# Performance work log

Hardware: AMD Instinct MI355X
Metric: run time of the kernel (lower is better)

The kernel has to match this reference:

```python
import jax, jax.numpy as jnp
import numpy as np

H = 16  # n_head

def _rotate_half(x):
    d = x.shape[-1] // 2
    return jnp.concatenate([-x[..., d:], x[..., :d]], axis=-1)

def setup_inputs() -> dict:
    key = jax.random.key(0)
    ks = jax.random.split(key, 12)
    b, t, f, h = 8, 1024, 1024, H
    d = f // h
    inp = {
        "query": jax.random.normal(ks[0], (b, t, f), jnp.float32),
        "key": jax.random.normal(ks[1], (b, t, f), jnp.float32),
        "value": jax.random.normal(ks[2], (b, t, f), jnp.float32),
    }
    # realistic rotary cos/sin, shape (t,1,1,d_k)
    inv_freq = 1.0 / (10000.0 ** (np.arange(0, d, 2, dtype=np.float32) / d))
    pos = np.arange(t, dtype=np.float32)[:, None] * inv_freq[None, :]  # (t, d/2)
    emb = np.concatenate([pos, pos], axis=-1)  # (t, d)
    inp["cos"] = jnp.asarray(np.cos(emb)).reshape(t, 1, 1, d)
    inp["sin"] = jnp.asarray(np.sin(emb)).reshape(t, 1, 1, d)
    inp["mask"] = jax.random.randint(ks[3], (b, t, t), 0, 2) > 0
    s = 1.0 / np.sqrt(f)
    inp["Wq"] = jax.random.normal(ks[4], (f, f), jnp.float32) * s
    inp["bq"] = jax.random.normal(ks[5], (f,), jnp.float32) * 0.02
    inp["Wk"] = jax.random.normal(ks[6], (f, f), jnp.float32) * s
    inp["bk"] = jax.random.normal(ks[7], (f,), jnp.float32) * 0.02
    inp["Wv"] = jax.random.normal(ks[8], (f, f), jnp.float32) * s
    inp["bv"] = jax.random.normal(ks[9], (f,), jnp.float32) * 0.02
    inp["Wo"] = jax.random.normal(ks[10], (f, f), jnp.float32) * s
    inp["bo"] = jax.random.normal(ks[11], (f,), jnp.float32) * 0.02
    return inp

def reference(query, key, value, cos, sin, mask, Wq, bq, Wk, bk, Wv, bv, Wo, bo):
    b, t, f = query.shape
    h = H
    d = f // h
    # RoPE applied pre-projection, per-head layout (b,t,h,d)
    c = cos.reshape(1, t, 1, d)  # broadcast over batch and heads
    s = sin.reshape(1, t, 1, d)
    qr = query.reshape(b, t, h, d)
    kr = key.reshape(b, t, h, d)
    qr = qr * c + _rotate_half(qr) * s
    kr = kr * c + _rotate_half(kr) * s
    q_in = qr.reshape(b, t, f)
    k_in = kr.reshape(b, t, f)
    # QKV projections (nn.Linear: x @ W.T + b), then split heads -> (b,h,t,d)
    q = (jnp.einsum('btf,gf->btg', q_in, Wq) + bq).reshape(b, t, h, d).transpose(0, 2, 1, 3)
    k = (jnp.einsum('btf,gf->btg', k_in, Wk) + bk).reshape(b, t, h, d).transpose(0, 2, 1, 3)
    v = (jnp.einsum('btf,gf->btg', value, Wv) + bv).reshape(b, t, h, d).transpose(0, 2, 1, 3)
    scores = jnp.einsum('bhqd,bhkd->bhqk', q, k) / jnp.sqrt(jnp.asarray(d, q.dtype))
    m = mask[:, None, :, :]  # (b,1,t,t)
    scores = jnp.where(m, jnp.asarray(-10000.0, scores.dtype), scores)
    attn = jax.nn.softmax(scores, axis=-1)
    attn = jnp.where(m, jnp.asarray(0.0, attn.dtype), attn)
    out = jnp.einsum('bhqk,bhkd->bhqd', attn, v)  # (b,h,t,d)
    out = out.transpose(0, 2, 1, 3).reshape(b, t, f)
    return jnp.einsum('btf,gf->btg', out, Wo) + bo
```

## Files before the change

kernel.cpp:

```cpp
#include <hip/hip_runtime.h>
#include <stdint.h>

typedef short short8 __attribute__((ext_vector_type(8)));
typedef float f32x4 __attribute__((ext_vector_type(4)));
typedef unsigned short ushort4v __attribute__((ext_vector_type(4)));
typedef unsigned int uint4v __attribute__((ext_vector_type(4)));
typedef unsigned long long u64;
typedef u64 u64x2 __attribute__((ext_vector_type(2)));

#if __has_builtin(__builtin_amdgcn_exp2f)
#define EXP2(x) __builtin_amdgcn_exp2f(x)
#else
#define EXP2(x) exp2f(x)
#endif

__device__ __forceinline__ unsigned short f2bf(float f) {
  union { float f; unsigned u; } v; v.f = f;
  unsigned r = v.u + 0x7fffu + ((v.u >> 16) & 1u);
  return (unsigned short)(r >> 16);
}

__device__ __forceinline__ unsigned cvt_pk_bf16(float lo, float hi) {
  unsigned r;
  asm("v_cvt_pk_bf16_f32 %0, %1, %2" : "=v"(r) : "v"(lo), "v"(hi));
  return r;
}

__device__ __forceinline__ void gld_lds16(const void* g, void* l) {
  __builtin_amdgcn_global_load_lds((const __attribute__((address_space(1))) void*)g,
                                   (__attribute__((address_space(3))) void*)l, 16, 0, 0);
}

__device__ __forceinline__ unsigned nib_compress(u64 x) {
  x = (x | (x >> 4))  & 0x00FF00FF00FF00FFull;
  x = (x | (x >> 8))  & 0x0000FFFF0000FFFFull;
  x = (x | (x >> 16));
  return (unsigned)x;
}

__device__ __forceinline__ void cast32(const float* __restrict__ src,
                                       unsigned short* __restrict__ dst) {
  const float4 a = *(const float4*)(src);
  const float4 b = *(const float4*)(src + 4);
  const float4 c = *(const float4*)(src + 8);
  const float4 d = *(const float4*)(src + 12);
  const float4 e = *(const float4*)(src + 16);
  const float4 f = *(const float4*)(src + 20);
  const float4 g = *(const float4*)(src + 24);
  const float4 h = *(const float4*)(src + 28);
  uint4v o0, o1, o2, o3;
  o0[0] = cvt_pk_bf16(a.x, a.y); o0[1] = cvt_pk_bf16(a.z, a.w);
  o0[2] = cvt_pk_bf16(b.x, b.y); o0[3] = cvt_pk_bf16(b.z, b.w);
  o1[0] = cvt_pk_bf16(c.x, c.y); o1[1] = cvt_pk_bf16(c.z, c.w);
  o1[2] = cvt_pk_bf16(d.x, d.y); o1[3] = cvt_pk_bf16(d.z, d.w);
  o2[0] = cvt_pk_bf16(e.x, e.y); o2[1] = cvt_pk_bf16(e.z, e.w);
  o2[2] = cvt_pk_bf16(f.x, f.y); o2[3] = cvt_pk_bf16(f.z, f.w);
  o3[0] = cvt_pk_bf16(g.x, g.y); o3[1] = cvt_pk_bf16(g.z, g.w);
  o3[2] = cvt_pk_bf16(h.x, h.y); o3[3] = cvt_pk_bf16(h.z, h.w);
  *(uint4v*)(dst)      = o0;
  *(uint4v*)(dst + 8)  = o1;
  *(uint4v*)(dst + 16) = o2;
  *(uint4v*)(dst + 24) = o3;
}

__global__ void prep_kernel(const float* __restrict__ q, const float* __restrict__ k,
                            const float* __restrict__ v,
                            const float* __restrict__ cs, const float* __restrict__ sn,
                            unsigned short* __restrict__ qo, unsigned short* __restrict__ ko,
                            unsigned short* __restrict__ vo,
                            const int* __restrict__ mask, u64* __restrict__ bits,
                            const float* __restrict__ s0, const float* __restrict__ s1,
                            const float* __restrict__ s2, const float* __restrict__ s3,
                            unsigned short* __restrict__ d0, unsigned short* __restrict__ d1,
                            unsigned short* __restrict__ d2, unsigned short* __restrict__ d3) {
  __shared__ unsigned mlds[256];
  const int tid = threadIdx.x;
  const int bx = blockIdx.x;
  if (bx < 1024) {
    const int idx  = bx * 256 + tid;
    const int half = idx & 1;
    const int row  = idx >> 1;
    const int t    = (row >> 4) & 1023;
    const size_t base = (size_t)row * 64 + half * 16;
    const int coff = t * 64 + half * 16;

    const float4 ca = *(const float4*)(cs + coff);
    const float4 cb = *(const float4*)(cs + coff + 4);
    const float4 cc = *(const float4*)(cs + coff + 8);
    const float4 cd = *(const float4*)(cs + coff + 12);
    const float4 sa = *(const float4*)(sn + coff);
    const float4 sb = *(const float4*)(sn + coff + 4);
    const float4 sc = *(const float4*)(sn + coff + 8);
    const float4 sd = *(const float4*)(sn + coff + 12);
    const float4 x0a = *(const float4*)(q + base);
    const float4 x0b = *(const float4*)(q + base + 4);
    const float4 x0c = *(const float4*)(q + base + 8);
    const float4 x0d = *(const float4*)(q + base + 12);
    const float4 x1a = *(const float4*)(q + base + 32);
    const float4 x1b = *(const float4*)(q + base + 36);
    const float4 x1c = *(const float4*)(q + base + 40);
    const float4 x1d = *(const float4*)(q + base + 44);
    const float4 y0a = *(const float4*)(k + base);
    const float4 y0b = *(const float4*)(k + base + 4);
    const float4 y0c = *(const float4*)(k + base + 8);
    const float4 y0d = *(const float4*)(k + base + 12);
    const float4 y1a = *(const float4*)(k + base + 32);
    const float4 y1b = *(const float4*)(k + base + 36);
    const float4 y1c = *(const float4*)(k + base + 40);
    const float4 y1d = *(const float4*)(k + base + 44);

    uint4v qlo0, qlo1, qhi0, qhi1;
    qlo0[0] = cvt_pk_bf16(x0a.x*ca.x - x1a.x*sa.x, x0a.y*ca.y - x1a.y*sa.y);
    qlo0[1] = cvt_pk_bf16(x0a.z*ca.z - x1a.z*sa.z, x0a.w*ca.w - x1a.w*sa.w);
    qlo0[2] = cvt_pk_bf16(x0b.x*cb.x - x1b.x*sb.x, x0b.y*cb.y - x1b.y*sb.y);
    qlo0[3] = cvt_pk_bf16(x0b.z*cb.z - x1b.z*sb.z, x0b.w*cb.w - x1b.w*sb.w);
    qlo1[0] = cvt_pk_bf16(x0c.x*cc.x - x1c.x*sc.x, x0c.y*cc.y - x1c.y*sc.y);
    qlo1[1] = cvt_pk_bf16(x0c.z*cc.z - x1c.z*sc.z, x0c.w*cc.w - x1c.w*sc.w);
    qlo1[2] = cvt_pk_bf16(x0d.x*cd.x - x1d.x*sd.x, x0d.y*cd.y - x1d.y*sd.y);
    qlo1[3] = cvt_pk_bf16(x0d.z*cd.z - x1d.z*sd.z, x0d.w*cd.w - x1d.w*sd.w);
    qhi0[0] = cvt_pk_bf16(x1a.x*ca.x + x0a.x*sa.x, x1a.y*ca.y + x0a.y*sa.y);
    qhi0[1] = cvt_pk_bf16(x1a.z*ca.z + x0a.z*sa.z, x1a.w*ca.w + x0a.w*sa.w);
    qhi0[2] = cvt_pk_bf16(x1b.x*cb.x + x0b.x*sb.x, x1b.y*cb.y + x0b.y*sb.y);
    qhi0[3] = cvt_pk_bf16(x1b.z*cb.z + x0b.z*sb.z, x1b.w*cb.w + x0b.w*sb.w);
    qhi1[0] = cvt_pk_bf16(x1c.x*cc.x + x0c.x*sc.x, x1c.y*cc.y + x0c.y*sc.y);
    qhi1[1] = cvt_pk_bf16(x1c.z*cc.z + x0c.z*sc.z, x1c.w*cc.w + x0c.w*sc.w);
    qhi1[2] = cvt_pk_bf16(x1d.x*cd.x + x0d.x*sd.x, x1d.y*cd.y + x0d.y*sd.y);
    qhi1[3] = cvt_pk_bf16(x1d.z*cd.z + x0d.z*sd.z, x1d.w*cd.w + x0d.w*sd.w);
    *(uint4v*)(qo + base)      = qlo0;
    *(uint4v*)(qo + base + 8)  = qlo1;
    *(uint4v*)(qo + base + 32) = qhi0;
    *(uint4v*)(qo + base + 40) = qhi1;

    uint4v klo0, klo1, khi0, khi1;
    klo0[0] = cvt_pk_bf16(y0a.x*ca.x - y1a.x*sa.x, y0a.y*ca.y - y1a.y*sa.y);
    klo0[1] = cvt_pk_bf16(y0a.z*ca.z - y1a.z*sa.z, y0a.w*ca.w - y1a.w*sa.w);
    klo0[2] = cvt_pk_bf16(y0b.x*cb.x - y1b.x*sb.x, y0b.y*cb.y - y1b.y*sb.y);
    klo0[3] = cvt_pk_bf16(y0b.z*cb.z - y1b.z*sb.z, y0b.w*cb.w - y1b.w*sb.w);
    klo1[0] = cvt_pk_bf16(y0c.x*cc.x - y1c.x*sc.x, y0c.y*cc.y - y1c.y*sc.y);
    klo1[1] = cvt_pk_bf16(y0c.z*cc.z - y1c.z*sc.z, y0c.w*cc.w - y1c.w*sc.w);
    klo1[2] = cvt_pk_bf16(y0d.x*cd.x - y1d.x*sd.x, y0d.y*cd.y - y1d.y*sd.y);
    klo1[3] = cvt_pk_bf16(y0d.z*cd.z - y1d.z*sd.z, y0d.w*cd.w - y1d.w*sd.w);
    khi0[0] = cvt_pk_bf16(y1a.x*ca.x + y0a.x*sa.x, y1a.y*ca.y + y0a.y*sa.y);
    khi0[1] = cvt_pk_bf16(y1a.z*ca.z + y0a.z*sa.z, y1a.w*ca.w + y0a.w*sa.w);
    khi0[2] = cvt_pk_bf16(y1b.x*cb.x + y0b.x*sb.x, y1b.y*cb.y + y0b.y*sb.y);
    khi0[3] = cvt_pk_bf16(y1b.z*cb.z + y0b.z*sb.z, y1b.w*cb.w + y0b.w*sb.w);
    khi1[0] = cvt_pk_bf16(y1c.x*cc.x + y0c.x*sc.x, y1c.y*cc.y + y0c.y*sc.y);
    khi1[1] = cvt_pk_bf16(y1c.z*cc.z + y0c.z*sc.z, y1c.w*cc.w + y0c.w*sc.w);
    khi1[2] = cvt_pk_bf16(y1d.x*cd.x + y0d.x*sd.x, y1d.y*cd.y + y0d.y*sd.y);
    khi1[3] = cvt_pk_bf16(y1d.z*cd.z + y0d.z*sd.z, y1d.w*cd.w + y0d.w*sd.w);
    *(uint4v*)(ko + base)      = klo0;
    *(uint4v*)(ko + base + 8)  = klo1;
    *(uint4v*)(ko + base + 32) = khi0;
    *(uint4v*)(ko + base + 40) = khi1;
  } else if (bx < 2048) {
    const size_t off = ((size_t)(bx - 1024) * 256 + tid) * 32;
    cast32(v + off, vo + off);
  } else if (bx < 2560) {
    const int idx2 = bx - 2048;
    const int m = idx2 >> 7;
    const float* src = (m == 0) ? s0 : (m == 1) ? s1 : (m == 2) ? s2 : s3;
    unsigned short* dst = (m == 0) ? d0 : (m == 1) ? d1 : (m == 2) ? d2 : d3;
    const size_t off = ((size_t)(idx2 & 127) * 256 + tid) * 32;
    cast32(src + off, dst + off);
  } else {
    const int wave = tid >> 6, lane = tid & 63;
    const int mrow = (bx - 2560) * 4 + wave;
    const int* mp = mask + (size_t)mrow * 1024 + lane * 16;
    const int4 a0 = *(const int4*)(mp);
    const int4 a1 = *(const int4*)(mp + 4);
    const int4 a2 = *(const int4*)(mp + 8);
    const int4 a3 = *(const int4*)(mp + 12);
    const unsigned n0 = (a0.x!=0?1u:0u)|(a0.y!=0?2u:0u)|(a0.z!=0?4u:0u)|(a0.w!=0?8u:0u);
    const unsigned n1 = (a1.x!=0?1u:0u)|(a1.y!=0?2u:0u)|(a1.z!=0?4u:0u)|(a1.w!=0?8u:0u);
    const unsigned n2 = (a2.x!=0?1u:0u)|(a2.y!=0?2u:0u)|(a2.z!=0?4u:0u)|(a2.w!=0?8u:0u);
    const unsigned n3 = (a3.x!=0?1u:0u)|(a3.y!=0?2u:0u)|(a3.z!=0?4u:0u)|(a3.w!=0?8u:0u);
    mlds[wave * 64 + lane] = n0 | (n1 << 8) | (n2 << 16) | (n3 << 24);
    if (lane < 16) {
      const u64x2 x = ((const u64x2*)mlds)[wave * 16 + lane];
      const u64 w = (u64)nib_compress(x[0]) | ((u64)nib_compress(x[1]) << 32);
      bits[(size_t)mrow * 16 + lane] = w;
    }
  }
}

__global__ __launch_bounds__(256, 4) void gemm_qkv(
    const unsigned short* __restrict__ Aq, const unsigned short* __restrict__ Ak,
    const unsigned short* __restrict__ Av,
    const unsigned short* __restrict__ Bq, const unsigned short* __restrict__ Bk,
    const unsigned short* __restrict__ Bv,
    const float* __restrict__ bq, const float* __restrict__ bk, const float* __restrict__ bv,
    unsigned short* __restrict__ Cq, unsigned short* __restrict__ Ck,
    unsigned short* __restrict__ Cv) {
  constexpr int K = 1024;
  const int z = blockIdx.z;
  const unsigned short* A  = (z == 0) ? Aq : (z == 1) ? Ak : Av;
  const unsigned short* Bw = (z == 0) ? Bq : (z == 1) ? Bk : Bv;
  const float* bias        = (z == 0) ? bq : (z == 1) ? bk : bv;
  unsigned short* Co       = (z == 0) ? Cq : (z == 1) ? Ck : Cv;
  const float scale = (z == 0) ? 0.18033688f : 1.0f;

  const int tid = threadIdx.x;
  const int wave = tid >> 6, lane = tid & 63;
  const int m0 = blockIdx.x * 128, n0 = blockIdx.y * 128;
  __shared__ unsigned short Asm[128 * 64];
  __shared__ unsigned short Bsm[128 * 64];
  f32x4 acc[4][4] = {};
  const int wr = (wave >> 1) * 64, wc = (wave & 1) * 64;
  const int ld_row = lane >> 3;
  const int ld_col = ((lane & 7) ^ ld_row) * 8;
  const int fr = lane & 15, g = lane >> 4;
  const int fr7 = fr & 7;

  for (int k0 = 0; k0 < K; k0 += 64) {
#pragma unroll
    for (int j = 0; j < 4; ++j) {
      const int c = j * 4 + wave;
      gld_lds16(A  + (size_t)(m0 + 8 * c + ld_row) * K + k0 + ld_col, &Asm[c * 512]);
      gld_lds16(Bw + (size_t)(n0 + 8 * c + ld_row) * K + k0 + ld_col, &Bsm[c * 512]);
    }
    __syncthreads();
#pragma unroll
    for (int ks = 0; ks < 2; ++ks) {
      const int ch = ((ks * 4 + g) ^ fr7) * 8;
      short8 af[4], bf[4];
#pragma unroll
      for (int i = 0; i < 4; ++i)
        af[i] = *(const short8*)&Asm[(wr + i * 16 + fr) * 64 + ch];
#pragma unroll
      for (int i = 0; i < 4; ++i)
        bf[i] = *(const short8*)&Bsm[(wc + i * 16 + fr) * 64 + ch];
#pragma unroll
      for (int i = 0; i < 4; ++i)
#pragma unroll
        for (int j = 0; j < 4; ++j)
          acc[i][j] = __builtin_amdgcn_mfma_f32_16x16x32_bf16(af[i], bf[j], acc[i][j], 0, 0, 0);
    }
    __syncthreads();
  }

#pragma unroll
  for (int i = 0; i < 4; ++i) {
    const int row_base = m0 + wr + i * 16 + g * 4;
#pragma unroll
    for (int j = 0; j < 4; ++j) {
      const int col = n0 + wc + j * 16 + fr;
      const float bval = bias[col];
      const int h_i = col >> 6, dd = col & 63;
      if (z < 2) {
#pragma unroll
        for (int r = 0; r < 4; ++r) {
          const int row = row_base + r;
          const int b_i = row >> 10, t_i = row & 1023;
          Co[((size_t)(b_i * 16 + h_i) * 1024 + t_i) * 64 + dd] = f2bf((acc[i][j][r] + bval) * scale);
        }
      } else {
#pragma unroll
        for (int r = 0; r < 4; ++r) {
          const int row = row_base + r;
          const int b_i = row >> 10, t_i = row & 1023;
          const int kk = t_i & 127;
          const int kp = ((kk >> 4) & 3) * 32 + ((kk >> 2) & 3) * 8 + ((kk >> 6) & 1) * 4 + (kk & 3);
          Co[((size_t)(b_i * 16 + h_i) * 64 + dd) * 1024 + (t_i & ~127) + kp] =
              f2bf((acc[i][j][r] + bval));
        }
      }
    }
  }
}

__global__ __launch_bounds__(256, 4) void gemm_o(
    const unsigned short* __restrict__ A, const unsigned short* __restrict__ Bw,
    const float* __restrict__ bias, float* __restrict__ C) {
  constexpr int K = 1024, N = 1024;
  const int tid = threadIdx.x;
  const int wave = tid >> 6, lane = tid & 63;
  const int m0 = blockIdx.x * 128, n0 = blockIdx.y * 128;
  __shared__ unsigned short Asm[128 * 64];
  __shared__ unsigned short Bsm[128 * 64];
  f32x4 acc[4][4] = {};
  const int wr = (wave >> 1) * 64, wc = (wave & 1) * 64;
  const int ld_row = lane >> 3;
  const int ld_col = ((lane & 7) ^ ld_row) * 8;
  const int fr = lane & 15, g = lane >> 4;
  const int fr7 = fr & 7;

  for (int k0 = 0; k0 < K; k0 += 64) {
#pragma unroll
    for (int j = 0; j < 4; ++j) {
      const int c = j * 4 + wave;
      gld_lds16(A  + (size_t)(m0 + 8 * c + ld_row) * K + k0 + ld_col, &Asm[c * 512]);
      gld_lds16(Bw + (size_t)(n0 + 8 * c + ld_row) * K + k0 + ld_col, &Bsm[c * 512]);
    }
    __syncthreads();
#pragma unroll
    for (int ks = 0; ks < 2; ++ks) {
      const int ch = ((ks * 4 + g) ^ fr7) * 8;
      short8 af[4], bf[4];
#pragma unroll
      for (int i = 0; i < 4; ++i)
        af[i] = *(const short8*)&Asm[(wr + i * 16 + fr) * 64 + ch];
#pragma unroll
      for (int i = 0; i < 4; ++i)
        bf[i] = *(const short8*)&Bsm[(wc + i * 16 + fr) * 64 + ch];
#pragma unroll
      for (int i = 0; i < 4; ++i)
#pragma unroll
        for (int j = 0; j < 4; ++j)
          acc[i][j] = __builtin_amdgcn_mfma_f32_16x16x32_bf16(af[i], bf[j], acc[i][j], 0, 0, 0);
    }
    __syncthreads();
  }

#pragma unroll
  for (int i = 0; i < 4; ++i) {
    const int row_base = m0 + wr + i * 16 + g * 4;
#pragma unroll
    for (int j = 0; j < 4; ++j) {
      const int col = n0 + wc + j * 16 + fr;
      const float bval = bias[col];
#pragma unroll
      for (int r = 0; r < 4; ++r)
        C[(size_t)(row_base + r) * N + col] = acc[i][j][r] + bval;
    }
  }
}

__global__ __launch_bounds__(256, 2) void flash_attn(
    const unsigned short* __restrict__ Qp, const unsigned short* __restrict__ Kp,
    const unsigned short* __restrict__ Vp, const u64* __restrict__ mbits,
    unsigned short* __restrict__ O) {
  const int bh = blockIdx.x & 127, b_i = bh >> 4, h_i = bh & 15;
  const int q0 = (blockIdx.x >> 7) * 128;
  const int tid = threadIdx.x, wave = tid >> 6, lane = tid & 63;
  const unsigned short* Qb = Qp + (size_t)bh * 65536;
  const unsigned short* Kb = Kp + (size_t)bh * 65536;
  const unsigned short* Vb = Vp + (size_t)bh * 65536;
  const u64* mb = mbits + (size_t)b_i * 16384;

  __shared__ unsigned short smem[32768];

  const int fr = lane & 15, g = lane >> 4, fr7 = fr & 7;
  const int shg = g * 4;
  const int qw = q0 + wave * 32;

  short8 qf[2][2];
#pragma unroll
  for (int mt = 0; mt < 2; ++mt)
#pragma unroll
    for (int ks = 0; ks < 2; ++ks)
      qf[mt][ks] = *(const short8*)&Qb[(size_t)(qw + mt * 16 + fr) * 64 + ks * 32 + g * 8];

  f32x4 o_acc[2][4] = {};
  f32x4 o_l[2] = {};
  const short8 ones = {0x3F80, 0x3F80, 0x3F80, 0x3F80, 0x3F80, 0x3F80, 0x3F80, 0x3F80};

  const int kld_row = lane >> 3;
  const int kld_col = ((lane & 7) ^ kld_row) * 8;
  const int vld_row = lane >> 4;
  const int vld_r7w = 4 * (wave & 1) + vld_row;
  const int vld_col = ((lane & 15) ^ vld_r7w) * 8;

#define STAGE(P, KT)                                                                     \
  do {                                                                                   \
    _Pragma("unroll")                                                                    \
    for (int j = 0; j < 4; ++j) {                                                        \
      const int c = j * 4 + wave;                                                        \
      gld_lds16(Kb + (size_t)((KT) + 8 * c + kld_row) * 64 + kld_col,                    \
                &smem[(P) * 16384 + 8192 + c * 512]);                                    \
      gld_lds16(Vb + (size_t)(4 * c + vld_row) * 1024 + (KT) + vld_col,                  \
                &smem[(P) * 16384 + c * 512]);                                           \
    }                                                                                    \
  } while (0)

  u64x2 wv0 = *(const u64x2*)&mb[(size_t)(qw + fr) * 16];
  u64x2 wv1 = *(const u64x2*)&mb[(size_t)(qw + 16 + fr) * 16];
  STAGE(0, 0);
  int p = 0;
  for (int kt = 0; kt < 1024; kt += 128) {
    if (kt < 896) {
      STAGE(p ^ 1, kt + 128);
      asm volatile("s_waitcnt vmcnt(8)" ::: "memory");
    } else {
      asm volatile("s_waitcnt vmcnt(0)" ::: "memory");
    }
    __builtin_amdgcn_s_barrier();
    asm volatile("" ::: "memory");
    const unsigned short* Vsm = &smem[p * 16384];
    const unsigned short* Ksm = &smem[p * 16384 + 8192];

    f32x4 s_acc[2][8] = {};
#pragma unroll
    for (int ks = 0; ks < 2; ++ks) {
      const int ch = ((ks * 4 + g) ^ fr7) * 8;
      short8 kf[8];
#pragma unroll
      for (int nt = 0; nt < 8; ++nt)
        kf[nt] = *(const short8*)&Ksm[(nt * 16 + fr) * 64 + ch];
      __builtin_amdgcn_s_setprio(1);
#pragma unroll
      for (int mt = 0; mt < 2; ++mt)
#pragma unroll
        for (int nt = 0; nt < 8; ++nt)
          s_acc[mt][nt] = __builtin_amdgcn_mfma_f32_16x16x32_bf16(kf[nt], qf[mt][ks], s_acc[mt][nt], 0, 0, 0);
      __builtin_amdgcn_s_setprio(0);
    }

    short8 pf[2][4];
#pragma unroll
    for (int mt = 0; mt < 2; ++mt) {
      const u64 sa = (mt ? wv1[0] : wv0[0]) >> shg;
      const u64 sb = (mt ? wv1[1] : wv0[1]) >> shg;
#pragma unroll
      for (int ks2 = 0; ks2 < 4; ++ks2) {
        float e[8];
#pragma unroll
        for (int r = 0; r < 4; ++r) {
          float a = EXP2(s_acc[mt][ks2][r]);
          a = ((unsigned)(sa >> (ks2 * 16 + r)) & 1u) ? 0.0f : a;
          float b2 = EXP2(s_acc[mt][ks2 + 4][r]);
          b2 = ((unsigned)(sb >> (ks2 * 16 + r)) & 1u) ? 0.0f : b2;
          e[r] = a; e[4 + r] = b2;
        }
        uint4v pk;
        pk[0] = cvt_pk_bf16(e[0], e[1]);
        pk[1] = cvt_pk_bf16(e[2], e[3]);
        pk[2] = cvt_pk_bf16(e[4], e[5]);
        pk[3] = cvt_pk_bf16(e[6], e[7]);
        union { uint4v u; short8 s; } cv; cv.u = pk;
        pf[mt][ks2] = cv.s;
      }
    }

    {
      const int ktn = (kt + 128) & 1023;
      wv0 = *(const u64x2*)&mb[(size_t)(qw + fr) * 16 + (ktn >> 6)];
      wv1 = *(const u64x2*)&mb[(size_t)(qw + 16 + fr) * 16 + (ktn >> 6)];
    }

#pragma unroll
    for (int ks2 = 0; ks2 < 4; ++ks2) {
      const int cc = (ks2 * 4 + g) ^ fr7;
      short8 vf[4];
#pragma unroll
      for (int dt = 0; dt < 4; ++dt)
        vf[dt] = *(const short8*)&Vsm[(dt * 16 + fr) * 128 + cc * 8];
      __builtin_amdgcn_s_setprio(1);
#pragma unroll
      for (int mt = 0; mt < 2; ++mt) {
#pragma unroll
        for (int dt = 0; dt < 4; ++dt)
          o_acc[mt][dt] = __builtin_amdgcn_mfma_f32_16x16x32_bf16(pf[mt][ks2], vf[dt], o_acc[mt][dt], 0, 0, 0);
        o_l[mt] = __builtin_amdgcn_mfma_f32_16x16x32_bf16(pf[mt][ks2], ones, o_l[mt], 0, 0, 0);
      }
      __builtin_amdgcn_s_setprio(0);
    }
    asm volatile("" ::: "memory");
    __builtin_amdgcn_s_barrier();
    p ^= 1;
  }
#undef STAGE

#pragma unroll
  for (int mt = 0; mt < 2; ++mt) {
#pragma unroll
    for (int r = 0; r < 4; ++r) {
      const float inv_l = 1.0f / o_l[mt][r];
      const int qrow = qw + mt * 16 + g * 4 + r;
#pragma unroll
      for (int dt = 0; dt < 4; ++dt) {
        const int dcol = dt * 16 + fr;
        O[((size_t)(b_i * 1024 + qrow)) * 1024 + h_i * 64 + dcol] = f2bf(o_acc[mt][dt][r] * inv_l);
      }
    }
  }
}

extern "C" void kernel_launch(void* const* d_in, const int* in_sizes, int n_in,
                              void* d_out, int out_size, void* d_ws, size_t ws_size,
                              hipStream_t stream) {
  const float* query = (const float*)d_in[0];
  const float* key   = (const float*)d_in[1];
  const float* value = (const float*)d_in[2];
  const float* cosb  = (const float*)d_in[3];
  const float* sinb  = (const float*)d_in[4];
  const int*   mask  = (const int*)d_in[5];
  const float* Wq = (const float*)d_in[6];
  const float* bq = (const float*)d_in[7];
  const float* Wk = (const float*)d_in[8];
  const float* bk = (const float*)d_in[9];
  const float* Wv = (const float*)d_in[10];
  const float* bv = (const float*)d_in[11];
  const float* Wo = (const float*)d_in[12];
  const float* bo = (const float*)d_in[13];
  (void)in_sizes; (void)n_in; (void)out_size; (void)ws_size;

  char* ws = (char*)d_ws;
  const size_t MB = 1024 * 1024;
  unsigned short* q_in = (unsigned short*)(ws);
  unsigned short* k_in = (unsigned short*)(ws + 16 * MB);
  unsigned short* v_bf = (unsigned short*)(ws + 32 * MB);
  unsigned short* Qp   = (unsigned short*)(ws + 48 * MB);
  unsigned short* Kp   = (unsigned short*)(ws + 64 * MB);
  unsigned short* Vp   = (unsigned short*)(ws + 80 * MB);
  unsigned short* Wqb  = (unsigned short*)(ws + 96 * MB);
  unsigned short* Wkb  = (unsigned short*)(ws + 98 * MB);
  unsigned short* Wvb  = (unsigned short*)(ws + 100 * MB);
  unsigned short* Wob  = (unsigned short*)(ws + 102 * MB);
  u64*            mbits= (u64*)(ws + 104 * MB);
  unsigned short* attn = q_in;

  prep_kernel<<<4608, 256, 0, stream>>>(query, key, value, cosb, sinb, q_in, k_in, v_bf,
                                        mask, mbits, Wq, Wk, Wv, Wo, Wqb, Wkb, Wvb, Wob);

  dim3 blk(256);
  gemm_qkv<<<dim3(64, 8, 3), blk, 0, stream>>>(q_in, k_in, v_bf, Wqb, Wkb, Wvb,
                                               bq, bk, bv, Qp, Kp, Vp);
  flash_attn<<<1024, blk, 0, stream>>>(Qp, Kp, Vp, mbits, attn);
  gemm_o<<<dim3(64, 8), blk, 0, stream>>>(attn, Wob, bo, (float*)d_out);
}
```

Measured before the change: 339.9 us.

## Double-buffer LDS tiles in QKV and output GEMMs with async prefetch

Both projection GEMMs now keep two LDS stages and issue the global-to-LDS loads for the next K tile before computing on the current one. Partial vmcnt waits and raw s_barrier replace the full __syncthreads, and setprio raises wave priority around the MFMA block. This is meant to hide global load latency behind matrix math. In exchange LDS use doubles, so occupancy is lowered to 2 blocks per CU, and the hand-counted vmcnt(8) has to match the number of outstanding loads issued per stage.

Measured after the change: 336.6 us. Within noise of the previous version (-0.9%).

```diff
diff --git a/kernel.cpp b/kernel.cpp
--- a/kernel.cpp
+++ b/kernel.cpp
@@ -183,7 +183,7 @@
   }
 }
 
-__global__ __launch_bounds__(256, 4) void gemm_qkv(
+__global__ __launch_bounds__(256, 2) void gemm_qkv(
     const unsigned short* __restrict__ Aq, const unsigned short* __restrict__ Ak,
     const unsigned short* __restrict__ Av,
     const unsigned short* __restrict__ Bq, const unsigned short* __restrict__ Bk,
@@ -202,8 +202,8 @@
   const int tid = threadIdx.x;
   const int wave = tid >> 6, lane = tid & 63;
   const int m0 = blockIdx.x * 128, n0 = blockIdx.y * 128;
-  __shared__ unsigned short Asm[128 * 64];
-  __shared__ unsigned short Bsm[128 * 64];
+  __shared__ unsigned short Asm[2][128 * 64];
+  __shared__ unsigned short Bsm[2][128 * 64];
   f32x4 acc[4][4] = {};
   const int wr = (wave >> 1) * 64, wc = (wave & 1) * 64;
   const int ld_row = lane >> 3;
@@ -211,32 +211,50 @@
   const int fr = lane & 15, g = lane >> 4;
   const int fr7 = fr & 7;
 
+#define GSTAGE(P, K0)                                                                    \
+  do {                                                                                   \
+    _Pragma("unroll")                                                                    \
+    for (int j = 0; j < 4; ++j) {                                                        \
+      const int c = j * 4 + wave;                                                        \
+      gld_lds16(A  + (size_t)(m0 + 8 * c + ld_row) * K + (K0) + ld_col, &Asm[P][c * 512]); \
+      gld_lds16(Bw + (size_t)(n0 + 8 * c + ld_row) * K + (K0) + ld_col, &Bsm[P][c * 512]); \
+    }                                                                                    \
+  } while (0)
+
+  GSTAGE(0, 0);
+  int p = 0;
   for (int k0 = 0; k0 < K; k0 += 64) {
-#pragma unroll
-    for (int j = 0; j < 4; ++j) {
-      const int c = j * 4 + wave;
-      gld_lds16(A  + (size_t)(m0 + 8 * c + ld_row) * K + k0 + ld_col, &Asm[c * 512]);
-      gld_lds16(Bw + (size_t)(n0 + 8 * c + ld_row) * K + k0 + ld_col, &Bsm[c * 512]);
-    }
-    __syncthreads();
+    if (k0 < K - 64) {
+      GSTAGE(p ^ 1, k0 + 64);
+      asm volatile("s_waitcnt vmcnt(8)" ::: "memory");
+    } else {
+      asm volatile("s_waitcnt vmcnt(0)" ::: "memory");
+    }
+    __builtin_amdgcn_s_barrier();
+    asm volatile("" ::: "memory");
 #pragma unroll
     for (int ks = 0; ks < 2; ++ks) {
       const int ch = ((ks * 4 + g) ^ fr7) * 8;
       short8 af[4], bf[4];
 #pragma unroll
       for (int i = 0; i < 4; ++i)
-        af[i] = *(const short8*)&Asm[(wr + i * 16 + fr) * 64 + ch];
+        af[i] = *(const short8*)&Asm[p][(wr + i * 16 + fr) * 64 + ch];
 #pragma unroll
       for (int i = 0; i < 4; ++i)
-        bf[i] = *(const short8*)&Bsm[(wc + i * 16 + fr) * 64 + ch];
+        bf[i] = *(const short8*)&Bsm[p][(wc + i * 16 + fr) * 64 + ch];
+      __builtin_amdgcn_s_setprio(1);
 #pragma unroll
       for (int i = 0; i < 4; ++i)
 #pragma unroll
         for (int j = 0; j < 4; ++j)
           acc[i][j] = __builtin_amdgcn_mfma_f32_16x16x32_bf16(af[i], bf[j], acc[i][j], 0, 0, 0);
-    }
-    __syncthreads();
-  }
+      __builtin_amdgcn_s_setprio(0);
+    }
+    asm volatile("" ::: "memory");
+    __builtin_amdgcn_s_barrier();
+    p ^= 1;
+  }
+#undef GSTAGE
 
 #pragma unroll
   for (int i = 0; i < 4; ++i) {
@@ -268,15 +286,15 @@
   }
 }
 
-__global__ __launch_bounds__(256, 4) void gemm_o(
+__global__ __launch_bounds__(256, 2) void gemm_o(
     const unsigned short* __restrict__ A, const unsigned short* __restrict__ Bw,
     const float* __restrict__ bias, float* __restrict__ C) {
   constexpr int K = 1024, N = 1024;
   const int tid = threadIdx.x;
   const int wave = tid >> 6, lane = tid & 63;
   const int m0 = blockIdx.x * 128, n0 = blockIdx.y * 128;
-  __shared__ unsigned short Asm[128 * 64];
-  __shared__ unsigned short Bsm[128 * 64];
+  __shared__ unsigned short Asm[2][128 * 64];
+  __shared__ unsigned short Bsm[2][128 * 64];
   f32x4 acc[4][4] = {};
   const int wr = (wave >> 1) * 64, wc = (wave & 1) * 64;
   const int ld_row = lane >> 3;
@@ -284,32 +302,50 @@
   const int fr = lane & 15, g = lane >> 4;
   const int fr7 = fr & 7;
 
+#define GSTAGE(P, K0)                                                                    \
+  do {                                                                                   \
+    _Pragma("unroll")                                                                    \
+    for (int j = 0; j < 4; ++j) {                                                        \
+      const int c = j * 4 + wave;                                                        \
+      gld_lds16(A  + (size_t)(m0 + 8 * c + ld_row) * K + (K0) + ld_col, &Asm[P][c * 512]); \
+      gld_lds16(Bw + (size_t)(n0 + 8 * c + ld_row) * K + (K0) + ld_col, &Bsm[P][c * 512]); \
+    }                                                                                    \
+  } while (0)
+
+  GSTAGE(0, 0);
+  int p = 0;
   for (int k0 = 0; k0 < K; k0 += 64) {
-#pragma unroll
-    for (int j = 0; j < 4; ++j) {
-      const int c = j * 4 + wave;
-      gld_lds16(A  + (size_t)(m0 + 8 * c + ld_row) * K + k0 + ld_col, &Asm[c * 512]);
-      gld_lds16(Bw + (size_t)(n0 + 8 * c + ld_row) * K + k0 + ld_col, &Bsm[c * 512]);
-    }
-    __syncthreads();
+    if (k0 < K - 64) {
+      GSTAGE(p ^ 1, k0 + 64);
+      asm volatile("s_waitcnt vmcnt(8)" ::: "memory");
+    } else {
+      asm volatile("s_waitcnt vmcnt(0)" ::: "memory");
+    }
+    __builtin_amdgcn_s_barrier();
+    asm volatile("" ::: "memory");
 #pragma unroll
     for (int ks = 0; ks < 2; ++ks) {
       const int ch = ((ks * 4 + g) ^ fr7) * 8;
       short8 af[4], bf[4];
 #pragma unroll
       for (int i = 0; i < 4; ++i)
-        af[i] = *(const short8*)&Asm[(wr + i * 16 + fr) * 64 + ch];
+        af[i] = *(const short8*)&Asm[p][(wr + i * 16 + fr) * 64 + ch];
 #pragma unroll
       for (int i = 0; i < 4; ++i)
-        bf[i] = *(const short8*)&Bsm[(wc + i * 16 + fr) * 64 + ch];
+        bf[i] = *(const short8*)&Bsm[p][(wc + i * 16 + fr) * 64 + ch];
+      __builtin_amdgcn_s_setprio(1);
 #pragma unroll
       for (int i = 0; i < 4; ++i)
 #pragma unroll
         for (int j = 0; j < 4; ++j)
           acc[i][j] = __builtin_amdgcn_mfma_f32_16x16x32_bf16(af[i], bf[j], acc[i][j], 0, 0, 0);
-    }
-    __syncthreads();
-  }
+      __builtin_amdgcn_s_setprio(0);
+    }
+    asm volatile("" ::: "memory");
+    __builtin_amdgcn_s_barrier();
+    p ^= 1;
+  }
+#undef GSTAGE
 
 #pragma unroll
   for (int i = 0; i < 4; ++i) {
```
